# Performance work log

Measured on AMD Instinct MI355X. Metric: run time of the kernel, lower is better.

Reference implementation:

```python
import jax, jax.numpy as jnp
import numpy as np

B, N, E = 16, 1000, 16000        # graphs, nodes/graph, edges/graph
H1, C1 = 8, 128                  # conv1 heads, per-head channels (hidden_size)
EMB, HID = 64, 128               # embed_size, mlp hidden_size


def gat_conv(x, ei, W, att_src, att_dst, bias, heads, concat):
    """PyG GATConv (eval mode, self-loops already in ei). x: [Ntot, Fin]."""
    Ntot = x.shape[0]
    C = W.shape[1] // heads
    h = (x @ W).reshape(Ntot, heads, C)                  # [Ntot, H, C]
    a_src = jnp.einsum('nhc,hc->nh', h, att_src)          # [Ntot, H]
    a_dst = jnp.einsum('nhc,hc->nh', h, att_dst)
    src, dst = ei[0], ei[1]
    alpha = jax.nn.leaky_relu(a_src[src] + a_dst[dst], 0.2)   # [Etot, H]
    # segment softmax over destination nodes (every node has a self loop)
    amax = jax.ops.segment_max(alpha, dst, num_segments=Ntot)
    ea = jnp.exp(alpha - amax[dst])
    denom = jax.ops.segment_sum(ea, dst, num_segments=Ntot)
    alpha = ea / denom[dst]
    msg = h[src] * alpha[:, :, None]                      # [Etot, H, C]
    out = jax.ops.segment_sum(msg, dst, num_segments=Ntot)   # [Ntot, H, C]
    out = out.reshape(Ntot, heads * C) if concat else out.mean(axis=1)
    return out + bias


def setup_inputs():
    key = jax.random.key(0)
    k = jax.random.split(key, 16)
    g = lambda kk, sh: (jax.random.normal(kk, sh, jnp.float32) * 0.1)
    return {
        'actions': jax.random.normal(k[0], (B, N, 2), jnp.float32),
        'node_features': jax.random.normal(k[1], (B, 1, N), jnp.float32),
        'edge_index': jax.random.randint(k[2], (B, 2, E), 0, N, dtype=jnp.int32),
        # conv1: GATConv(3, C1, heads=H1, concat=True)
        'W1': g(k[3], (3, H1 * C1)),
        'att_src1': g(k[4], (H1, C1)),
        'att_dst1': g(k[5], (H1, C1)),
        'b1': g(k[6], (H1 * C1,)),
        # conv2: GATConv(H1*C1, EMB, heads=1, concat=False)
        'W2': g(k[7], (H1 * C1, EMB)),
        'att_src2': g(k[8], (1, EMB)),
        'att_dst2': g(k[9], (1, EMB)),
        'b2': g(k[10], (EMB,)),
        # MLP head
        'mlp_w1': g(k[11], (N * EMB, HID)),
        'mlp_b1': jnp.zeros((HID,), jnp.float32),
        'mlp_w2': g(k[12], (HID, HID)),
        'mlp_b2': jnp.zeros((HID,), jnp.float32),
        'out_w': g(k[13], (HID, N)),
        'out_b': jnp.zeros((N,), jnp.float32),
    }


def reference(actions, node_features, edge_index, W1, att_src1, att_dst1, b1,
              W2, att_src2, att_dst2, b2, mlp_w1, mlp_b1, mlp_w2, mlp_b2,
              out_w, out_b):
    Bn, _, Nn = node_features.shape
    nf = node_features.astype(jnp.float32).squeeze(1)                 # [B, N]
    x = jnp.stack([actions[:, :, 0], actions[:, :, 1], nf], axis=2)   # [B, N, 3]
    x = x.reshape(Bn * Nn, 3)
    # batch-offset edge index, then faithful row-major reshape to [2, B*E]
    ei = (edge_index + (jnp.arange(Bn) * Nn)[:, None, None]).reshape(2, -1)
    loops = jnp.broadcast_to(jnp.arange(Bn * Nn)[None, :], (2, Bn * Nn))
    ei = jnp.concatenate([ei, loops], axis=1)
    # eval mode: dropouts are no-ops
    x = jax.nn.elu(gat_conv(x, ei, W1, att_src1, att_dst1, b1, H1, True))
    x = jax.nn.elu(gat_conv(x, ei, W2, att_src2, att_dst2, b2, 1, False))
    x = x.reshape(Bn, Nn * EMB)
    x = jax.nn.relu(x @ mlp_w1 + mlp_b1)
    x = jax.nn.relu(x @ mlp_w2 + mlp_b2)
    return jax.nn.sigmoid(x @ out_w + out_b)                          # [B, N]
```

## Files before the change

kernel.cpp:

```cpp
#include <hip/hip_runtime.h>
#include <math.h>

#define NB 16
#define NN 1000
#define NT 16000
#define NE 16000
#define EBASE 256000
#define ETOT 272000
#define F1 1024
#define EMB 64
#define HID 128
#define KTOT 64000
#define MLP1B 1024
#define NREP 8
#define CAP 96
#define PBASE 0xAAAAAAAAu

typedef unsigned short ushort_t;
typedef unsigned int uint_t;
typedef __attribute__((ext_vector_type(8))) _Float16 half8;
typedef __attribute__((ext_vector_type(4))) float float4_;
typedef __attribute__((ext_vector_type(2))) float float2_;
typedef __attribute__((ext_vector_type(2))) uint_t uint2_;

__device__ __forceinline__ int src_of(const int* ei, int j) {
    if (j < EBASE) return ei[j] + (j / 32000) * 1000;
    return j - EBASE;
}
__device__ __forceinline__ int dst_of(const int* ei, int j) {
    if (j < EBASE) return ei[EBASE + j] + (8 + j / 32000) * 1000;
    return j - EBASE;
}

__device__ __forceinline__ float lrelu02(float r) { return r >= 0.f ? r : 0.2f * r; }
__device__ __forceinline__ float elu1(float v)    { return v > 0.f ? v : expm1f(v); }
__device__ __forceinline__ ushort_t f2h(float f) {
    _Float16 h = (_Float16)f;
    union { _Float16 h; ushort_t u; } c; c.h = h; return c.u;
}

__global__ __launch_bounds__(256) void k_prepfill(
    const float* __restrict__ actions, const float* __restrict__ nf,
    const float* __restrict__ W1, const float* __restrict__ as1w, const float* __restrict__ ad1w,
    const float* __restrict__ W2, const int* __restrict__ ei,
    float* __restrict__ x4, float* __restrict__ as1, float* __restrict__ ad1,
    ushort_t* __restrict__ w2f, int* __restrict__ cnt, int* __restrict__ esrc) {
    __shared__ float tile[64][65];
    __shared__ float was[24], wad[24];
    int bid = blockIdx.x, t = threadIdx.x;

    if (bid < 63) {
        if (t < 24) {
            int k = t / 8, h = t % 8;
            float ss = 0.f, dd = 0.f;
            for (int c = 0; c < 128; ++c) {
                float w = W1[k * F1 + h * 128 + c];
                ss += w * as1w[h * 128 + c];
                dd += w * ad1w[h * 128 + c];
            }
            was[t] = ss; wad[t] = dd;
        }
        __syncthreads();
        int n = bid * 256 + t;
        if (n < NT) {
            float x0 = actions[n * 2 + 0];
            float x1v = actions[n * 2 + 1];
            float x2v = nf[n];
            float4_ xv = {x0, x1v, x2v, 0.f};
            *(float4_*)(x4 + (size_t)n * 4) = xv;
            #pragma unroll
            for (int h = 0; h < 8; ++h) {
                as1[n * 8 + h] = x0 * was[h] + x1v * was[8 + h] + x2v * was[16 + h];
                ad1[n * 8 + h] = x0 * wad[h] + x1v * wad[8 + h] + x2v * wad[16 + h];
            }
        }
    } else if (bid < 79) {
        int k0 = (bid - 63) * 64;
        int c = t & 63, g = t >> 6;
        for (int r = g; r < 64; r += 4)
            tile[r][c] = W2[(size_t)(k0 + r) * 64 + c];
        __syncthreads();
        for (int q = t; q < 512; q += 256) {
            int t4 = q >> 7, ksl = (q >> 6) & 1, l8 = q & 63;
            int kg = l8 >> 4, mrow = l8 & 15;
            int n = t4 * 16 + mrow;
            int kloc = ksl * 32 + kg * 8;
            size_t base = (((size_t)t4 * 32 + (k0 >> 5) + ksl) * 64 + l8) * 8;
            #pragma unroll
            for (int j = 0; j < 8; ++j)
                w2f[base + j] = f2h(tile[kloc + j][n]);
        }
    } else {
        int j = (bid - 79) * 256 + t;
        if (j < ETOT) {
            int dv = dst_of(ei, j);
            uint_t old = (uint_t)atomicAdd(&cnt[dv], 1);
            int slot = (int)(old - PBASE);
            if (slot >= 0 && slot < CAP)
                esrc[(size_t)dv * CAP + slot] = src_of(ei, j);
        }
    }
}

__global__ __launch_bounds__(256) void k_conv1h2(
    const int* __restrict__ cnt, const int* __restrict__ esrc, const float* __restrict__ x4,
    const float* __restrict__ as1, const float* __restrict__ ad1,
    const float* __restrict__ W1, const float* __restrict__ b1,
    const ushort_t* __restrict__ w2f,
    const float* __restrict__ as2w, const float* __restrict__ ad2w,
    float* __restrict__ h2, float* __restrict__ a2s, float* __restrict__ a2d) {
    __shared__ ushort_t x1t[16][1032];
    __shared__ float smb[16][8][3];
    __shared__ float a2p[4][16][2];
    int t = threadIdx.x, wave = t >> 6, lane = t & 63;

    float4_ w0 = *(const float4_*)(W1 + t * 4);
    float4_ w1r = *(const float4_*)(W1 + F1 + t * 4);
    float4_ w2r = *(const float4_*)(W1 + 2 * F1 + t * 4);
    float4_ bb = *(const float4_*)(b1 + t * 4);

    int g = lane >> 4, lg = lane & 15, eslot = lg >> 3, h = lg & 7;
    int nd0 = wave * 4 + g;
    int d = blockIdx.x * 16 + nd0;
    int cn = (int)((uint_t)cnt[d] - PBASE);
    cn = (cn < CAP) ? cn : CAP;
    const int* ep = esrc + (size_t)d * CAP;
    float adv = ad1[d * 8 + h];
    float den = 0.f, s0 = 0.f, s1 = 0.f, s2 = 0.f;
    for (int e = eslot; e < cn; e += 2) {
        int s = ep[e];
        float ea = __expf(lrelu02(as1[s * 8 + h] + adv));
        float4_ xv = *(const float4_*)(x4 + (size_t)s * 4);
        den += ea; s0 += ea * xv.x; s1 += ea * xv.y; s2 += ea * xv.z;
    }
    den += __shfl_xor(den, 8, 64);
    s0  += __shfl_xor(s0, 8, 64);
    s1  += __shfl_xor(s1, 8, 64);
    s2  += __shfl_xor(s2, 8, 64);
    if (eslot == 0) {
        float inv = 1.f / den;
        smb[nd0][h][0] = s0 * inv;
        smb[nd0][h][1] = s1 * inv;
        smb[nd0][h][2] = s2 * inv;
    }
    __syncthreads();

    int hh = t >> 5;
    #pragma unroll 4
    for (int nd = 0; nd < 16; ++nd) {
        float c0 = smb[nd][hh][0], c1 = smb[nd][hh][1], c2 = smb[nd][hh][2];
        float v0 = c0 * w0.x + c1 * w1r.x + c2 * w2r.x + bb.x;
        float v1 = c0 * w0.y + c1 * w1r.y + c2 * w2r.y + bb.y;
        float v2 = c0 * w0.z + c1 * w1r.z + c2 * w2r.z + bb.z;
        float v3 = c0 * w0.w + c1 * w1r.w + c2 * w2r.w + bb.w;
        v0 = elu1(v0); v1 = elu1(v1); v2 = elu1(v2); v3 = elu1(v3);
        uint2_ pk;
        pk.x = (uint_t)f2h(v0) | ((uint_t)f2h(v1) << 16);
        pk.y = (uint_t)f2h(v2) | ((uint_t)f2h(v3) << 16);
        *(uint2_*)(&x1t[nd][t * 4]) = pk;
    }
    __syncthreads();

    int mrow = lane & 15, kg = lane >> 4;
    const ushort_t* bp = w2f + ((size_t)wave * 32 * 64 + lane) * 8;
    float4_ acc = {0.f, 0.f, 0.f, 0.f};
    #pragma unroll 8
    for (int ks = 0; ks < 32; ++ks) {
        half8 a = *(const half8*)(&x1t[mrow][kg * 8 + ks * 32]);
        half8 b = *(const half8*)(bp + (size_t)ks * 512);
        acc = __builtin_amdgcn_mfma_f32_16x16x32_f16(a, b, acc, 0, 0, 0);
    }
    int row0 = blockIdx.x * 16;
    #pragma unroll
    for (int r = 0; r < 4; ++r)
        h2[(size_t)(row0 + kg * 4 + r) * EMB + wave * 16 + mrow] = acc[r];

    float sw = as2w[wave * 16 + mrow], dw = ad2w[wave * 16 + mrow];
    float ps[4], pd[4];
    #pragma unroll
    for (int r = 0; r < 4; ++r) { ps[r] = acc[r] * sw; pd[r] = acc[r] * dw; }
    #pragma unroll
    for (int st = 1; st < 16; st <<= 1) {
        #pragma unroll
        for (int r = 0; r < 4; ++r) {
            ps[r] += __shfl_xor(ps[r], st, 64);
            pd[r] += __shfl_xor(pd[r], st, 64);
        }
    }
    if (mrow == 0) {
        #pragma unroll
        for (int r = 0; r < 4; ++r) {
            a2p[wave][kg * 4 + r][0] = ps[r];
            a2p[wave][kg * 4 + r][1] = pd[r];
        }
    }
    __syncthreads();
    if (t < 16) {
        float ss = a2p[0][t][0] + a2p[1][t][0] + a2p[2][t][0] + a2p[3][t][0];
        float dd = a2p[0][t][1] + a2p[1][t][1] + a2p[2][t][1] + a2p[3][t][1];
        a2s[row0 + t] = ss; a2d[row0 + t] = dd;
    }
}

__global__ __launch_bounds__(256) void k_conv2(
    const int* __restrict__ cnt, const int* __restrict__ esrc, const float* __restrict__ h2,
    const float* __restrict__ a2s, const float* __restrict__ a2d, const float* __restrict__ b2,
    float* __restrict__ x2) {
    int t = threadIdx.x;
    int wave = t >> 6, lane = t & 63;
    int d = blockIdx.x * 4 + wave;
    int cn = (int)((uint_t)cnt[d] - PBASE);
    cn = (cn < CAP) ? cn : CAP;
    const int* ep = esrc + (size_t)d * CAP;
    float adv = a2d[d];
    int eg = lane >> 4, c4 = (lane & 15) * 4;

    float den = 0.f;
    float4_ acc = {0.f, 0.f, 0.f, 0.f};
    for (int e = eg; e < cn; e += 4) {
        int s = ep[e];
        float ea = __expf(lrelu02(a2s[s] + adv));
        float4_ hv = *(const float4_*)(h2 + (size_t)s * EMB + c4);
        den += ea;
        acc.x += ea * hv.x; acc.y += ea * hv.y; acc.z += ea * hv.z; acc.w += ea * hv.w;
    }
    #pragma unroll
    for (int st = 16; st < 64; st <<= 1) {
        den   += __shfl_xor(den, st, 64);
        acc.x += __shfl_xor(acc.x, st, 64);
        acc.y += __shfl_xor(acc.y, st, 64);
        acc.z += __shfl_xor(acc.z, st, 64);
        acc.w += __shfl_xor(acc.w, st, 64);
    }
    if (eg == 0) {
        float inv = 1.f / den;
        float4_ o;
        o.x = elu1(acc.x * inv + b2[c4 + 0]);
        o.y = elu1(acc.y * inv + b2[c4 + 1]);
        o.z = elu1(acc.z * inv + b2[c4 + 2]);
        o.w = elu1(acc.w * inv + b2[c4 + 3]);
        *(float4_*)(x2 + (size_t)d * EMB + c4) = o;
    }
}

__global__ __launch_bounds__(256) void k_mlp1(const float* __restrict__ x2,
                                              const float* __restrict__ w1,
                                              float* __restrict__ y1rep) {
    __shared__ float red[NB * HID];
    int t = threadIdx.x;
    int wave = t >> 6, lane = t & 63;
    int j2 = lane * 2;
    float2_ acc[NB];
    #pragma unroll
    for (int b = 0; b < NB; ++b) acc[b] = (float2_){0.f, 0.f};

    for (int k = blockIdx.x * 4 + wave; k < KTOT; k += MLP1B * 4) {
        int kk = __builtin_amdgcn_readfirstlane(k);
        float2_ w = *(const float2_*)(w1 + (size_t)kk * HID + j2);
        const float* xr = x2 + kk;
        #pragma unroll
        for (int b = 0; b < NB; ++b) {
            float xv = xr[(size_t)b * KTOT];
            acc[b].x += xv * w.x;
            acc[b].y += xv * w.y;
        }
    }
    for (int w = 0; w < 4; ++w) {
        if (wave == w) {
            #pragma unroll
            for (int b = 0; b < NB; ++b) {
                if (w == 0) {
                    red[b * HID + j2]     = acc[b].x;
                    red[b * HID + j2 + 1] = acc[b].y;
                } else {
                    red[b * HID + j2]     += acc[b].x;
                    red[b * HID + j2 + 1] += acc[b].y;
                }
            }
        }
        __syncthreads();
    }
    float* yp = y1rep + (size_t)(blockIdx.x & (NREP - 1)) * (NB * HID);
    for (int idx = t; idx < NB * HID; idx += 256)
        atomicAdd(&yp[idx], red[idx]);
}

__global__ __launch_bounds__(256) void k_tail(
    const float* __restrict__ y1rep, const float* __restrict__ mb1,
    const float* __restrict__ mw2, const float* __restrict__ mb2,
    const float* __restrict__ ow, const float* __restrict__ ob,
    float* __restrict__ out) {
    __shared__ float y1[NB * HID];
    __shared__ float y2s[NB * HID];
    __shared__ float oacc[16][16][17];
    int t = threadIdx.x;

    for (int idx = t; idx < NB * HID; idx += 256) {
        float s = 0.f;
        #pragma unroll
        for (int r = 0; r < NREP; ++r)
            s += y1rep[(size_t)r * (NB * HID) + idx];
        y1[idx] = fmaxf(s + mb1[idx & 127], 0.f);
    }
    __syncthreads();

    #pragma unroll
    for (int i = 0; i < 8; ++i) {
        int o = t + i * 256;
        int b = o >> 7, j = o & 127;
        float acc = mb2[j];
        for (int k = 0; k < HID; ++k) acc += y1[b * HID + k] * mw2[k * HID + j];
        y2s[o] = fmaxf(acc, 0.f);
    }
    __syncthreads();

    int nl = t & 15, jg = t >> 4;
    int n = blockIdx.x * 16 + nl;
    float acc[NB];
    #pragma unroll
    for (int b = 0; b < NB; ++b) acc[b] = 0.f;
    if (n < NN) {
        #pragma unroll
        for (int jj = 0; jj < 8; ++jj) {
            int j = jg * 8 + jj;
            float w = ow[j * NN + n];
            #pragma unroll
            for (int b = 0; b < NB; ++b) acc[b] += y2s[b * HID + j] * w;
        }
    }
    #pragma unroll
    for (int b = 0; b < NB; ++b) oacc[jg][nl][b] = acc[b];
    __syncthreads();
    int b = t >> 4, nl2 = t & 15;
    float s = 0.f;
    #pragma unroll
    for (int q = 0; q < 16; ++q) s += oacc[q][nl2][b];
    int n2 = blockIdx.x * 16 + nl2;
    if (n2 < NN)
        out[b * NN + n2] = 1.f / (1.f + __expf(-(s + ob[n2])));
}

extern "C" void kernel_launch(void* const* d_in, const int* in_sizes, int n_in,
                              void* d_out, int out_size, void* d_ws, size_t ws_size,
                              hipStream_t stream) {
    const float* actions = (const float*)d_in[0];
    const float* nf      = (const float*)d_in[1];
    const int*   ei      = (const int*)d_in[2];
    const float* W1      = (const float*)d_in[3];
    const float* as1w    = (const float*)d_in[4];
    const float* ad1w    = (const float*)d_in[5];
    const float* b1      = (const float*)d_in[6];
    const float* W2      = (const float*)d_in[7];
    const float* as2w    = (const float*)d_in[8];
    const float* ad2w    = (const float*)d_in[9];
    const float* b2      = (const float*)d_in[10];
    const float* mw1     = (const float*)d_in[11];
    const float* mb1     = (const float*)d_in[12];
    const float* mw2     = (const float*)d_in[13];
    const float* mb2     = (const float*)d_in[14];
    const float* ow      = (const float*)d_in[15];
    const float* ob      = (const float*)d_in[16];
    float* out = (float*)d_out;

    float* f = (float*)d_ws;
    float* x4    = f;  f += (size_t)NT * 4;
    float* h2    = f;  f += (size_t)NT * EMB;
    float* x2    = f;  f += (size_t)NT * EMB;
    float* as1   = f;  f += NT * 8;
    float* ad1   = f;  f += NT * 8;
    float* a2s   = f;  f += NT;
    float* a2d   = f;  f += NT;
    float* y1rep = f;  f += (size_t)NREP * NB * HID;
    ushort_t* w2f = (ushort_t*)f;
    int* ip = (int*)(w2f + 65536);
    int* cnt  = ip; ip += NT;
    int* esrc = ip; ip += (size_t)NT * CAP;

    k_prepfill<<<1142, 256, 0, stream>>>(actions, nf, W1, as1w, ad1w, W2, ei,
                                         x4, as1, ad1, w2f, cnt, esrc);
    k_conv1h2<<<NT / 16, 256, 0, stream>>>(cnt, esrc, x4, as1, ad1, W1, b1, w2f,
                                           as2w, ad2w, h2, a2s, a2d);
    k_conv2<<<NT / 4, 256, 0, stream>>>(cnt, esrc, h2, a2s, a2d, b2, x2);
    k_mlp1<<<MLP1B, 256, 0, stream>>>(x2, mw1, y1rep);
    k_tail<<<64, 256, 0, stream>>>(y1rep, mb1, mw2, mb2, ow, ob, out);
}
```

Baseline: 201.1 us.

## Fuse conv2 aggregation with first MLP layer per node index

```diff
diff --git a/kernel.cpp b/kernel.cpp
--- a/kernel.cpp
+++ b/kernel.cpp
@@ -10,8 +10,6 @@
 #define F1 1024
 #define EMB 64
 #define HID 128
-#define KTOT 64000
-#define MLP1B 1024
 #define NREP 8
 #define CAP 96
 #define PBASE 0xAAAAAAAAu
@@ -202,87 +200,80 @@
     }
 }
 
-__global__ __launch_bounds__(256) void k_conv2(
+__global__ __launch_bounds__(256) void k_conv2mlp1(
     const int* __restrict__ cnt, const int* __restrict__ esrc, const float* __restrict__ h2,
     const float* __restrict__ a2s, const float* __restrict__ a2d, const float* __restrict__ b2,
-    float* __restrict__ x2) {
+    const float* __restrict__ w1, float* __restrict__ y1rep) {
+    __shared__ float x2s[EMB * NB];
+    __shared__ float y1p[2 * NB * HID];
     int t = threadIdx.x;
     int wave = t >> 6, lane = t & 63;
-    int d = blockIdx.x * 4 + wave;
-    int cn = (int)((uint_t)cnt[d] - PBASE);
-    cn = (cn < CAP) ? cn : CAP;
-    const int* ep = esrc + (size_t)d * CAP;
-    float adv = a2d[d];
+    int n = blockIdx.x;
     int eg = lane >> 4, c4 = (lane & 15) * 4;
 
-    float den = 0.f;
-    float4_ acc = {0.f, 0.f, 0.f, 0.f};
-    for (int e = eg; e < cn; e += 4) {
-        int s = ep[e];
-        float ea = __expf(lrelu02(a2s[s] + adv));
-        float4_ hv = *(const float4_*)(h2 + (size_t)s * EMB + c4);
-        den += ea;
-        acc.x += ea * hv.x; acc.y += ea * hv.y; acc.z += ea * hv.z; acc.w += ea * hv.w;
-    }
-    #pragma unroll
-    for (int st = 16; st < 64; st <<= 1) {
-        den   += __shfl_xor(den, st, 64);
-        acc.x += __shfl_xor(acc.x, st, 64);
-        acc.y += __shfl_xor(acc.y, st, 64);
-        acc.z += __shfl_xor(acc.z, st, 64);
-        acc.w += __shfl_xor(acc.w, st, 64);
-    }
-    if (eg == 0) {
-        float inv = 1.f / den;
-        float4_ o;
-        o.x = elu1(acc.x * inv + b2[c4 + 0]);
-        o.y = elu1(acc.y * inv + b2[c4 + 1]);
-        o.z = elu1(acc.z * inv + b2[c4 + 2]);
-        o.w = elu1(acc.w * inv + b2[c4 + 3]);
-        *(float4_*)(x2 + (size_t)d * EMB + c4) = o;
-    }
-}
-
-__global__ __launch_bounds__(256) void k_mlp1(const float* __restrict__ x2,
-                                              const float* __restrict__ w1,
-                                              float* __restrict__ y1rep) {
-    __shared__ float red[NB * HID];
-    int t = threadIdx.x;
-    int wave = t >> 6, lane = t & 63;
-    int j2 = lane * 2;
-    float2_ acc[NB];
-    #pragma unroll
-    for (int b = 0; b < NB; ++b) acc[b] = (float2_){0.f, 0.f};
-
-    for (int k = blockIdx.x * 4 + wave; k < KTOT; k += MLP1B * 4) {
-        int kk = __builtin_amdgcn_readfirstlane(k);
-        float2_ w = *(const float2_*)(w1 + (size_t)kk * HID + j2);
-        const float* xr = x2 + kk;
-        #pragma unroll
-        for (int b = 0; b < NB; ++b) {
-            float xv = xr[(size_t)b * KTOT];
-            acc[b].x += xv * w.x;
-            acc[b].y += xv * w.y;
-        }
-    }
-    for (int w = 0; w < 4; ++w) {
-        if (wave == w) {
+    for (int nd = 0; nd < 4; ++nd) {
+        int b = wave * 4 + nd;
+        int d = b * NN + n;
+        int cn = (int)((uint_t)cnt[d] - PBASE);
+        cn = (cn < CAP) ? cn : CAP;
+        const int* ep = esrc + (size_t)d * CAP;
+        float adv = a2d[d];
+        float den = 0.f;
+        float4_ acc = {0.f, 0.f, 0.f, 0.f};
+        for (int e = eg; e < cn; e += 4) {
+            int s = ep[e];
+            float ea = __expf(lrelu02(a2s[s] + adv));
+            float4_ hv = *(const float4_*)(h2 + (size_t)s * EMB + c4);
+            den += ea;
+            acc.x += ea * hv.x; acc.y += ea * hv.y; acc.z += ea * hv.z; acc.w += ea * hv.w;
+        }
+        #pragma unroll
+        for (int st = 16; st < 64; st <<= 1) {
+            den   += __shfl_xor(den, st, 64);
+            acc.x += __shfl_xor(acc.x, st, 64);
+            acc.y += __shfl_xor(acc.y, st, 64);
+            acc.z += __shfl_xor(acc.z, st, 64);
+            acc.w += __shfl_xor(acc.w, st, 64);
+        }
+        if (eg == 0) {
+            float inv = 1.f / den;
             #pragma unroll
-            for (int b = 0; b < NB; ++b) {
-                if (w == 0) {
-                    red[b * HID + j2]     = acc[b].x;
-                    red[b * HID + j2 + 1] = acc[b].y;
-                } else {
-                    red[b * HID + j2]     += acc[b].x;
-                    red[b * HID + j2 + 1] += acc[b].y;
-                }
-            }
-        }
-        __syncthreads();
-    }
+            for (int q = 0; q < 4; ++q)
+                x2s[(c4 + q) * NB + b] = elu1(acc[q] * inv + b2[c4 + q]);
+        }
+    }
+    __syncthreads();
+
+    int j = t & 127, kh = t >> 7;
+    float am[NB];
+    #pragma unroll
+    for (int b = 0; b < NB; ++b) am[b] = 0.f;
+    const float* wp = w1 + ((size_t)n * EMB + kh * 32) * HID + j;
+    #pragma unroll 4
+    for (int kk = 0; kk < 32; ++kk) {
+        float w = wp[(size_t)kk * HID];
+        const float* xr = x2s + (kh * 32 + kk) * NB;
+        float4_ xb0 = *(const float4_*)(xr);
+        float4_ xb1 = *(const float4_*)(xr + 4);
+        float4_ xb2 = *(const float4_*)(xr + 8);
+        float4_ xb3 = *(const float4_*)(xr + 12);
+        am[0] += xb0.x * w; am[1] += xb0.y * w; am[2] += xb0.z * w; am[3] += xb0.w * w;
+        am[4] += xb1.x * w; am[5] += xb1.y * w; am[6] += xb1.z * w; am[7] += xb1.w * w;
+        am[8] += xb2.x * w; am[9] += xb2.y * w; am[10] += xb2.z * w; am[11] += xb2.w * w;
+        am[12] += xb3.x * w; am[13] += xb3.y * w; am[14] += xb3.z * w; am[15] += xb3.w * w;
+    }
+    #pragma unroll
+    for (int b = 0; b < NB; ++b)
+        y1p[(kh * NB + b) * HID + j] = am[b];
+    __syncthreads();
+
     float* yp = y1rep + (size_t)(blockIdx.x & (NREP - 1)) * (NB * HID);
-    for (int idx = t; idx < NB * HID; idx += 256)
-        atomicAdd(&yp[idx], red[idx]);
+    #pragma unroll
+    for (int i = 0; i < 8; ++i) {
+        int idx = kh * 1024 + i * 128 + j;
+        float v = y1p[idx] + y1p[NB * HID + idx];
+        atomicAdd(&yp[idx], v);
+    }
 }
 
 __global__ __launch_bounds__(256) void k_tail(
@@ -365,7 +356,6 @@
     float* f = (float*)d_ws;
     float* x4    = f;  f += (size_t)NT * 4;
     float* h2    = f;  f += (size_t)NT * EMB;
-    float* x2    = f;  f += (size_t)NT * EMB;
     float* as1   = f;  f += NT * 8;
     float* ad1   = f;  f += NT * 8;
     float* a2s   = f;  f += NT;
@@ -380,7 +370,6 @@
                                          x4, as1, ad1, w2f, cnt, esrc);
     k_conv1h2<<<NT / 16, 256, 0, stream>>>(cnt, esrc, x4, as1, ad1, W1, b1, w2f,
                                            as2w, ad2w, h2, a2s, a2d);
-    k_conv2<<<NT / 4, 256, 0, stream>>>(cnt, esrc, h2, a2s, a2d, b2, x2);
-    k_mlp1<<<MLP1B, 256, 0, stream>>>(x2, mw1, y1rep);
+    k_conv2mlp1<<<NN, 256, 0, stream>>>(cnt, esrc, h2, a2s, a2d, b2, mw1, y1rep);
     k_tail<<<64, 256, 0, stream>>>(y1rep, mb1, mw2, mb2, ow, ob, out);
 }
```

New measurement: 194.9 us. 3.1% less time.
